# Optimization experiments

Measured on AMD Instinct MI355X. Metric: run time of the kernel, lower is better.

## Reference

```python
import jax, jax.numpy as jnp
import numpy as np

B, C, H, W = 4, 256, 64, 64
CQK = C // 8  # qk_downscale = 8


def setup_inputs() -> dict:
    key = jax.random.key(0)
    ks = jax.random.split(key, 4)
    scale = 0.02
    x = jax.random.normal(ks[0], (B, C, H, W), dtype=jnp.float32)
    Wq = jax.random.normal(ks[1], (CQK, C), dtype=jnp.float32) * scale
    bq = jnp.zeros((CQK,), dtype=jnp.float32)
    Wk = jax.random.normal(ks[2], (CQK, C), dtype=jnp.float32) * scale
    bk = jnp.zeros((CQK,), dtype=jnp.float32)
    Wv = jax.random.normal(ks[3], (C, C), dtype=jnp.float32) * scale
    bv = jnp.zeros((C,), dtype=jnp.float32)
    gamma = jnp.ones((1,), dtype=jnp.float32)
    return {"x": x, "Wq": Wq, "bq": bq, "Wk": Wk, "bk": bk,
            "Wv": Wv, "bv": bv, "gamma": gamma}


def reference(x, Wq, bq, Wk, bk, Wv, bv, gamma):
    b, c, h, w = x.shape
    n = h * w
    xf = x.reshape(b, c, n)                                   # [B,C,N]
    # 1x1 Conv1d == per-position linear projection
    q = jnp.einsum('oc,bcn->bon', Wq, xf) + bq[:, None]        # [B,C/8,N]
    k = jnp.einsum('oc,bcn->bon', Wk, xf) + bk[:, None]        # [B,C/8,N]
    v = jnp.einsum('oc,bcn->bon', Wv, xf) + bv[:, None]        # [B,C,N]
    # scores[b,i,j] = sum_c q[b,c,i] * k[b,c,j]  (bmm(q^T, k))
    scores = jnp.einsum('bci,bcj->bij', q, k)                  # [B,N,N]
    # softmax over dim=1 (the i / contracted axis) — SAGAN style, no 1/sqrt(d)
    attn = jax.nn.softmax(scores, axis=1)                      # [B,N,N]
    out = gamma * jnp.einsum('bcn,bnm->bcm', v, attn) + xf     # [B,C,N]
    return out.reshape(b, c, h, w)
```

## Files before the change

### kernel.cpp

```cpp
#include <hip/hip_runtime.h>
#include <stdint.h>

typedef __attribute__((ext_vector_type(8))) short short8;
typedef __attribute__((ext_vector_type(4))) float f32x4;
typedef __attribute__((ext_vector_type(4))) unsigned int u32x4;

#define MFMA16(a, b, c) __builtin_amdgcn_mfma_f32_16x16x32_bf16((a), (b), (c), 0, 0, 0)

#define GLOAD_LDS16(gsrc, ldst)                                                        \
    __builtin_amdgcn_global_load_lds(                                                  \
        (const __attribute__((address_space(1))) unsigned int*)(gsrc),                 \
        (__attribute__((address_space(3))) unsigned int*)(ldst), 16, 0, 0)

#define LOG2E 1.4426950408889634f

static __device__ __forceinline__ unsigned short f2bf(float f) {
    union { float f; unsigned int u; } v; v.f = f;
    unsigned int u = v.u;
    unsigned int r = 0x7fffu + ((u >> 16) & 1u);
    return (unsigned short)((u + r) >> 16);
}

static __device__ __forceinline__ float bf2f(unsigned short s) {
    union { unsigned int u; float f; } v; v.u = ((unsigned int)s) << 16;
    return v.f;
}

static __device__ __forceinline__ unsigned int cvt_pk_bf16(float lo, float hi) {
    unsigned int r;
    asm("v_cvt_pk_bf16_f32 %0, %1, %2" : "=v"(r) : "v"(lo), "v"(hi));
    return r;
}

__global__ __launch_bounds__(256) void k_prepw(const float* __restrict__ Wq,
                                               const float* __restrict__ Wk,
                                               const float* __restrict__ Wv,
                                               unsigned short* __restrict__ Wb) {
    const int i = (blockIdx.x * 256 + threadIdx.x) * 4;
    const float* src; int off;
    if (i < 8192)       { src = Wq; off = i; }
    else if (i < 16384) { src = Wk; off = i - 8192; }
    else                { src = Wv; off = i - 16384; }
    const float4 v = *(const float4*)(src + off);
    ushort4 o;
    o.x = f2bf(v.x); o.y = f2bf(v.y); o.z = f2bf(v.z); o.w = f2bf(v.w);
    *(ushort4*)(Wb + i) = o;
}

__global__ __launch_bounds__(256) void k_qkv(const float* __restrict__ x,
                                             const unsigned short* __restrict__ Wb,
                                             const float* __restrict__ bq,
                                             const float* __restrict__ bk,
                                             const float* __restrict__ bv,
                                             unsigned short* __restrict__ qT,
                                             unsigned short* __restrict__ kT,
                                             unsigned short* __restrict__ vp) {
    const int b = blockIdx.y;
    const int nt = blockIdx.x;
    const int h = blockIdx.z;
    const int lane = threadIdx.x & 63;
    const int wv = threadIdx.x >> 6;
    const int l15 = lane & 15, g = lane >> 4;
    const int n0 = nt * 64;
    const int nw = n0 + wv * 16;

    const float* xb = x + (size_t)b * 1048576;
    const float* xs = xb + (size_t)(g * 8) * 4096 + nw + l15;

    const unsigned short* Wqb = Wb;
    const unsigned short* Wkb = Wb + 8192;
    const unsigned short* Wvb = Wb + 16384 + h * 32768;

    f32x4 aqk[4] = {};
    f32x4 av[8] = {};

#pragma unroll 2
    for (int k0 = 0; k0 < 256; k0 += 32) {
        const float* xp = xs + (size_t)k0 * 4096;
        float xv[8];
#pragma unroll
        for (int j = 0; j < 8; ++j) xv[j] = xp[(size_t)j * 4096];
        const u32x4 ux = {cvt_pk_bf16(xv[0], xv[1]), cvt_pk_bf16(xv[2], xv[3]),
                          cvt_pk_bf16(xv[4], xv[5]), cvt_pk_bf16(xv[6], xv[7])};
        const short8 xa = __builtin_bit_cast(short8, ux);

        if (h == 0) {
#pragma unroll
            for (int ot = 0; ot < 4; ++ot) {
                const unsigned short* wr = (ot < 2) ? (Wqb + (size_t)(ot * 16 + l15) * 256)
                                                    : (Wkb + (size_t)((ot - 2) * 16 + l15) * 256);
                const short8 wb8 = *(const short8*)(wr + k0 + g * 8);
                aqk[ot] = MFMA16(xa, wb8, aqk[ot]);
            }
        }
#pragma unroll
        for (int ct = 0; ct < 8; ++ct) {
            const short8 wv8 = *(const short8*)(Wvb + (size_t)(ct * 16 + l15) * 256 + k0 + g * 8);
            av[ct] = MFMA16(wv8, xa, av[ct]);
        }
    }

    if (h == 0) {
#pragma unroll
        for (int ot = 0; ot < 4; ++ot) {
            const int o = (ot & 1) * 16 + l15;
            const float bias = (ot < 2) ? bq[o] : bk[o];
            const float sc = (ot < 2) ? LOG2E : 1.0f;
            unsigned short* dst = (ot < 2) ? qT : kT;
#pragma unroll
            for (int r = 0; r < 4; ++r) {
                const int n = nw + g * 4 + r;
                dst[((size_t)b * 4096 + n) * 32 + o] = f2bf((aqk[ot][r] + bias) * sc);
            }
        }
    }
    const int jp = ((wv >> 1) * 4 + (l15 >> 2)) * 8 + (wv & 1) * 4 + (l15 & 3);
#pragma unroll
    for (int ct = 0; ct < 8; ++ct)
#pragma unroll
        for (int r = 0; r < 4; ++r) {
            const int c = h * 128 + ct * 16 + g * 4 + r;
            vp[((size_t)b * 256 + c) * 4096 + n0 + jp] = f2bf(av[ct][r] + bv[c]);
        }
}

__global__ __launch_bounds__(256, 2) void k_attn(const unsigned short* __restrict__ qT,
                                                 const unsigned short* __restrict__ kT,
                                                 const unsigned short* __restrict__ vp,
                                                 unsigned short* __restrict__ Opart,
                                                 float* __restrict__ mll,
                                                 int ilen) {
    __shared__ __align__(16) unsigned short vlds[2 * 16384];

    const int b = blockIdx.y;
    const int mt = blockIdx.x;
    const int sp = blockIdx.z;
    const int tid = threadIdx.x;
    const int lane = tid & 63;
    const int wv = tid >> 6;
    const int l15 = lane & 15, g = lane >> 4;
    const int m_base = mt * 128 + wv * 32;
    const int i_start = sp * ilen;
    const int T = ilen >> 6;

    const unsigned short* qTb = qT + (size_t)b * 131072;
    const unsigned short* vpb = vp + (size_t)b * 1048576;

    const short8 qkB0 = *(const short8*)(kT + ((size_t)b * 4096 + m_base + l15) * 32 + g * 8);
    const short8 qkB1 = *(const short8*)(kT + ((size_t)b * 4096 + m_base + 16 + l15) * 32 + g * 8);

    const int jd = (lane & 7) ^ ((lane >> 3) & 7);
    const unsigned short* vsrc = vpb + (size_t)(64 * wv + (lane >> 3)) * 4096 + i_start + jd * 8;
    const int ldst0 = wv * 4096;

#define STAGE(bufsel, ioff)                                                             \
    do {                                                                                \
        _Pragma("unroll")                                                               \
        for (int s_ = 0; s_ < 8; ++s_)                                                  \
            GLOAD_LDS16(vsrc + (size_t)s_ * 32768 + (ioff),                             \
                        vlds + (bufsel) * 16384 + ldst0 + s_ * 512);                    \
    } while (0)

    const int rdA = l15 * 64 + ((g ^ (l15 & 7)) << 3);
    const int rdB = l15 * 64 + (((4 + g) ^ (l15 & 7)) << 3);

    const unsigned short* qp = qTb + (size_t)(i_start + l15) * 32 + g * 8;

    f32x4 oacc[16][2] = {};
    float l_acc0 = 0.0f, l_acc1 = 0.0f;
    const f32x4 zf = {0.f, 0.f, 0.f, 0.f};

    STAGE(0, 0);
    __syncthreads();

    for (int t = 0; t < T; ++t) {
        const int cur = t & 1;
        if (t + 1 < T) STAGE(cur ^ 1, (t + 1) * 64);

        const short8 a0 = *(const short8*)(qp);
        const short8 a1 = *(const short8*)(qp + 512);
        const short8 a2 = *(const short8*)(qp + 1024);
        const short8 a3 = *(const short8*)(qp + 1536);
        qp += 2048;
        f32x4 P[4][2];
        P[0][0] = MFMA16(a0, qkB0, zf); P[0][1] = MFMA16(a0, qkB1, zf);
        P[1][0] = MFMA16(a1, qkB0, zf); P[1][1] = MFMA16(a1, qkB1, zf);
        P[2][0] = MFMA16(a2, qkB0, zf); P[2][1] = MFMA16(a2, qkB1, zf);
        P[3][0] = MFMA16(a3, qkB0, zf); P[3][1] = MFMA16(a3, qkB1, zf);

        float s00 = 0.f, s01 = 0.f, s10 = 0.f, s11 = 0.f;
#pragma unroll
        for (int it = 0; it < 4; ++it)
#pragma unroll
            for (int r = 0; r < 4; ++r) {
                P[it][0][r] = exp2f(P[it][0][r]);
                P[it][1][r] = exp2f(P[it][1][r]);
                if (it < 2) { s00 += P[it][0][r]; s01 += P[it][1][r]; }
                else        { s10 += P[it][0][r]; s11 += P[it][1][r]; }
            }
        l_acc0 += s00 + s10;
        l_acc1 += s01 + s11;

        const u32x4 u00 = {cvt_pk_bf16(P[0][0][0], P[0][0][1]), cvt_pk_bf16(P[0][0][2], P[0][0][3]),
                           cvt_pk_bf16(P[1][0][0], P[1][0][1]), cvt_pk_bf16(P[1][0][2], P[1][0][3])};
        const u32x4 u01 = {cvt_pk_bf16(P[0][1][0], P[0][1][1]), cvt_pk_bf16(P[0][1][2], P[0][1][3]),
                           cvt_pk_bf16(P[1][1][0], P[1][1][1]), cvt_pk_bf16(P[1][1][2], P[1][1][3])};
        const u32x4 u10 = {cvt_pk_bf16(P[2][0][0], P[2][0][1]), cvt_pk_bf16(P[2][0][2], P[2][0][3]),
                           cvt_pk_bf16(P[3][0][0], P[3][0][1]), cvt_pk_bf16(P[3][0][2], P[3][0][3])};
        const u32x4 u11 = {cvt_pk_bf16(P[2][1][0], P[2][1][1]), cvt_pk_bf16(P[2][1][2], P[2][1][3]),
                           cvt_pk_bf16(P[3][1][0], P[3][1][1]), cvt_pk_bf16(P[3][1][2], P[3][1][3])};
        const short8 pb00 = __builtin_bit_cast(short8, u00);
        const short8 pb01 = __builtin_bit_cast(short8, u01);
        const short8 pb10 = __builtin_bit_cast(short8, u10);
        const short8 pb11 = __builtin_bit_cast(short8, u11);

        const unsigned short* vbase = vlds + cur * 16384;
        const unsigned short* pA = vbase + rdA;
        const unsigned short* pB = vbase + rdB;
        __builtin_amdgcn_s_setprio(1);
#pragma unroll
        for (int ct = 0; ct < 16; ++ct) {
            const short8 va0 = *(const short8*)(pA + ct * 1024);
            const short8 va1 = *(const short8*)(pB + ct * 1024);
            oacc[ct][0] = MFMA16(va0, pb00, oacc[ct][0]);
            oacc[ct][1] = MFMA16(va0, pb01, oacc[ct][1]);
            oacc[ct][0] = MFMA16(va1, pb10, oacc[ct][0]);
            oacc[ct][1] = MFMA16(va1, pb11, oacc[ct][1]);
        }
        __builtin_amdgcn_s_setprio(0);

        if (t + 1 < T) __syncthreads();
    }
#undef STAGE

    unsigned short* Ob = Opart + (size_t)(sp * 4 + b) * 1048576;
#pragma unroll
    for (int ct = 0; ct < 16; ++ct)
#pragma unroll
        for (int r = 0; r < 4; ++r) {
            const int c = ct * 16 + g * 4 + r;
            Ob[(size_t)c * 4096 + m_base + l15]      = f2bf(oacc[ct][0][r]);
            Ob[(size_t)c * 4096 + m_base + 16 + l15] = f2bf(oacc[ct][1][r]);
        }
    float l0 = l_acc0, l1 = l_acc1;
    l0 += __shfl_xor(l0, 16); l0 += __shfl_xor(l0, 32);
    l1 += __shfl_xor(l1, 16); l1 += __shfl_xor(l1, 32);
    if (lane < 16) {
        const size_t mi = (size_t)(sp * 4 + b) * 4096 + m_base + l15;
        mll[mi]      = l0;
        mll[mi + 16] = l1;
    }
}

__global__ __launch_bounds__(256) void k_combine(const unsigned short* __restrict__ Opart,
                                                 const float* __restrict__ mll,
                                                 const float* __restrict__ x,
                                                 const float* __restrict__ gamma,
                                                 float* __restrict__ out, int S) {
    const size_t e0 = ((size_t)blockIdx.x * 256 + threadIdx.x) * 8;
    const int m0 = (int)(e0 & 4095);
    const int b = (int)(e0 >> 20);

    float L[8] = {}, O[8] = {};
    for (int s = 0; s < S; ++s) {
        const size_t base = (size_t)(s * 4 + b) * 4096 + m0;
        const float4 la = *(const float4*)(mll + base);
        const float4 lc = *(const float4*)(mll + base + 4);
        const short8 op = *(const short8*)(Opart + (size_t)s * 4194304 + e0);
        L[0] += la.x; O[0] += bf2f((unsigned short)op[0]);
        L[1] += la.y; O[1] += bf2f((unsigned short)op[1]);
        L[2] += la.z; O[2] += bf2f((unsigned short)op[2]);
        L[3] += la.w; O[3] += bf2f((unsigned short)op[3]);
        L[4] += lc.x; O[4] += bf2f((unsigned short)op[4]);
        L[5] += lc.y; O[5] += bf2f((unsigned short)op[5]);
        L[6] += lc.z; O[6] += bf2f((unsigned short)op[6]);
        L[7] += lc.w; O[7] += bf2f((unsigned short)op[7]);
    }

    const float g0 = gamma[0];
    const float4 x0 = *(const float4*)(x + e0);
    const float4 x1 = *(const float4*)(x + e0 + 4);
    float4 o0, o1;
    o0.x = g0 * O[0] / L[0] + x0.x; o0.y = g0 * O[1] / L[1] + x0.y;
    o0.z = g0 * O[2] / L[2] + x0.z; o0.w = g0 * O[3] / L[3] + x0.w;
    o1.x = g0 * O[4] / L[4] + x1.x; o1.y = g0 * O[5] / L[5] + x1.y;
    o1.z = g0 * O[6] / L[6] + x1.z; o1.w = g0 * O[7] / L[7] + x1.w;
    *(float4*)(out + e0) = o0;
    *(float4*)(out + e0 + 4) = o1;
}

extern "C" void kernel_launch(void* const* d_in, const int* in_sizes, int n_in,
                              void* d_out, int out_size, void* d_ws, size_t ws_size,
                              hipStream_t stream) {
    (void)in_sizes; (void)n_in; (void)out_size;
    const float* x     = (const float*)d_in[0];
    const float* Wq    = (const float*)d_in[1];
    const float* bq    = (const float*)d_in[2];
    const float* Wk    = (const float*)d_in[3];
    const float* bk    = (const float*)d_in[4];
    const float* Wv    = (const float*)d_in[5];
    const float* bv    = (const float*)d_in[6];
    const float* gamma = (const float*)d_in[7];
    float* out = (float*)d_out;

    unsigned short* qT = (unsigned short*)d_ws;
    unsigned short* kT = qT + (size_t)4 * 4096 * 32;
    unsigned short* vp = kT + (size_t)4 * 4096 * 32;
    unsigned short* Wb = vp + (size_t)4 * 256 * 4096;
    unsigned short* Opart = Wb + 81920;

    const size_t base_el = 2 * (size_t)4 * 4096 * 32 + (size_t)4 * 256 * 4096 + 81920;
    auto need = [&](int s) {
        return (base_el + (size_t)s * 4194304) * 2 + (size_t)s * 16384 * 4;
    };
    const int S = (need(4) <= ws_size) ? 4 : (need(2) <= ws_size) ? 2 : 1;
    float* mll = (float*)(Opart + (size_t)S * 4194304);

    k_prepw<<<dim3(80), 256, 0, stream>>>(Wq, Wk, Wv, Wb);
    k_qkv<<<dim3(64, 4, 2), 256, 0, stream>>>(x, Wb, bq, bk, bv, qT, kT, vp);
    k_attn<<<dim3(32, 4, S), 256, 0, stream>>>(qT, kT, vp, Opart, mll, 4096 / S);
    k_combine<<<dim3(2048), 256, 0, stream>>>(Opart, mll, x, gamma, out, S);
}
```

Measured before the change: 93.19 us.

## Software-pipeline QK/softmax of next tile under PV MFMAs of current tile

Restructures the attention loop into a two-stage software pipeline, unrolled by two with ping-pong P buffers. The QK MFMAs and exp/pack for tile t+1 are issued around the PV MFMAs of tile t, so the exp work can overlap matrix-core work. It also drops the s_setprio calls. The loop now assumes T is even, and keeping two packed P sets live raises register pressure.

```diff
diff --git a/kernel.cpp b/kernel.cpp
--- a/kernel.cpp
+++ b/kernel.cpp
@@ -164,74 +164,95 @@
     const int rdA = l15 * 64 + ((g ^ (l15 & 7)) << 3);
     const int rdB = l15 * 64 + (((4 + g) ^ (l15 & 7)) << 3);
 
-    const unsigned short* qp = qTb + (size_t)(i_start + l15) * 32 + g * 8;
-
     f32x4 oacc[16][2] = {};
     float l_acc0 = 0.0f, l_acc1 = 0.0f;
     const f32x4 zf = {0.f, 0.f, 0.f, 0.f};
 
+#define QK_TILE(TT, P)                                                                  \
+    do {                                                                                \
+        const unsigned short* q_ = qTb + (size_t)(i_start + (TT) * 64 + l15) * 32 + g * 8; \
+        const short8 a0_ = *(const short8*)(q_);                                        \
+        const short8 a1_ = *(const short8*)(q_ + 512);                                  \
+        const short8 a2_ = *(const short8*)(q_ + 1024);                                 \
+        const short8 a3_ = *(const short8*)(q_ + 1536);                                 \
+        P[0][0] = MFMA16(a0_, qkB0, zf); P[0][1] = MFMA16(a0_, qkB1, zf);               \
+        P[1][0] = MFMA16(a1_, qkB0, zf); P[1][1] = MFMA16(a1_, qkB1, zf);               \
+        P[2][0] = MFMA16(a2_, qkB0, zf); P[2][1] = MFMA16(a2_, qkB1, zf);               \
+        P[3][0] = MFMA16(a3_, qkB0, zf); P[3][1] = MFMA16(a3_, qkB1, zf);               \
+    } while (0)
+
+#define SM_PACK(P, PB)                                                                  \
+    do {                                                                                \
+        float s00 = 0.f, s01 = 0.f, s10 = 0.f, s11 = 0.f;                               \
+        _Pragma("unroll")                                                               \
+        for (int it = 0; it < 4; ++it)                                                  \
+            _Pragma("unroll")                                                           \
+            for (int r = 0; r < 4; ++r) {                                               \
+                P[it][0][r] = exp2f(P[it][0][r]);                                       \
+                P[it][1][r] = exp2f(P[it][1][r]);                                       \
+                if (it < 2) { s00 += P[it][0][r]; s01 += P[it][1][r]; }                 \
+                else        { s10 += P[it][0][r]; s11 += P[it][1][r]; }                 \
+            }                                                                           \
+        l_acc0 += s00 + s10;                                                            \
+        l_acc1 += s01 + s11;                                                            \
+        const u32x4 u0_ = {cvt_pk_bf16(P[0][0][0], P[0][0][1]), cvt_pk_bf16(P[0][0][2], P[0][0][3]), \
+                           cvt_pk_bf16(P[1][0][0], P[1][0][1]), cvt_pk_bf16(P[1][0][2], P[1][0][3])}; \
+        const u32x4 u1_ = {cvt_pk_bf16(P[0][1][0], P[0][1][1]), cvt_pk_bf16(P[0][1][2], P[0][1][3]), \
+                           cvt_pk_bf16(P[1][1][0], P[1][1][1]), cvt_pk_bf16(P[1][1][2], P[1][1][3])}; \
+        const u32x4 u2_ = {cvt_pk_bf16(P[2][0][0], P[2][0][1]), cvt_pk_bf16(P[2][0][2], P[2][0][3]), \
+                           cvt_pk_bf16(P[3][0][0], P[3][0][1]), cvt_pk_bf16(P[3][0][2], P[3][0][3])}; \
+        const u32x4 u3_ = {cvt_pk_bf16(P[2][1][0], P[2][1][1]), cvt_pk_bf16(P[2][1][2], P[2][1][3]), \
+                           cvt_pk_bf16(P[3][1][0], P[3][1][1]), cvt_pk_bf16(P[3][1][2], P[3][1][3])}; \
+        PB[0] = __builtin_bit_cast(short8, u0_);                                        \
+        PB[1] = __builtin_bit_cast(short8, u1_);                                        \
+        PB[2] = __builtin_bit_cast(short8, u2_);                                        \
+        PB[3] = __builtin_bit_cast(short8, u3_);                                        \
+    } while (0)
+
+#define PV_TILE(CUR, PB)                                                                \
+    do {                                                                                \
+        const unsigned short* pA_ = vlds + (CUR) * 16384 + rdA;                         \
+        const unsigned short* pB_ = vlds + (CUR) * 16384 + rdB;                         \
+        _Pragma("unroll")                                                               \
+        for (int ct = 0; ct < 16; ++ct) {                                               \
+            const short8 va0_ = *(const short8*)(pA_ + ct * 1024);                      \
+            const short8 va1_ = *(const short8*)(pB_ + ct * 1024);                      \
+            oacc[ct][0] = MFMA16(va0_, PB[0], oacc[ct][0]);                             \
+            oacc[ct][1] = MFMA16(va0_, PB[1], oacc[ct][1]);                             \
+            oacc[ct][0] = MFMA16(va1_, PB[2], oacc[ct][0]);                             \
+            oacc[ct][1] = MFMA16(va1_, PB[3], oacc[ct][1]);                             \
+        }                                                                               \
+    } while (0)
+
+    short8 pbA[4], pbB[4];
+    f32x4 Pt[4][2];
+
     STAGE(0, 0);
+    QK_TILE(0, Pt);
+    SM_PACK(Pt, pbA);
     __syncthreads();
 
-    for (int t = 0; t < T; ++t) {
-        const int cur = t & 1;
-        if (t + 1 < T) STAGE(cur ^ 1, (t + 1) * 64);
-
-        const short8 a0 = *(const short8*)(qp);
-        const short8 a1 = *(const short8*)(qp + 512);
-        const short8 a2 = *(const short8*)(qp + 1024);
-        const short8 a3 = *(const short8*)(qp + 1536);
-        qp += 2048;
-        f32x4 P[4][2];
-        P[0][0] = MFMA16(a0, qkB0, zf); P[0][1] = MFMA16(a0, qkB1, zf);
-        P[1][0] = MFMA16(a1, qkB0, zf); P[1][1] = MFMA16(a1, qkB1, zf);
-        P[2][0] = MFMA16(a2, qkB0, zf); P[2][1] = MFMA16(a2, qkB1, zf);
-        P[3][0] = MFMA16(a3, qkB0, zf); P[3][1] = MFMA16(a3, qkB1, zf);
-
-        float s00 = 0.f, s01 = 0.f, s10 = 0.f, s11 = 0.f;
-#pragma unroll
-        for (int it = 0; it < 4; ++it)
-#pragma unroll
-            for (int r = 0; r < 4; ++r) {
-                P[it][0][r] = exp2f(P[it][0][r]);
-                P[it][1][r] = exp2f(P[it][1][r]);
-                if (it < 2) { s00 += P[it][0][r]; s01 += P[it][1][r]; }
-                else        { s10 += P[it][0][r]; s11 += P[it][1][r]; }
-            }
-        l_acc0 += s00 + s10;
-        l_acc1 += s01 + s11;
-
-        const u32x4 u00 = {cvt_pk_bf16(P[0][0][0], P[0][0][1]), cvt_pk_bf16(P[0][0][2], P[0][0][3]),
-                           cvt_pk_bf16(P[1][0][0], P[1][0][1]), cvt_pk_bf16(P[1][0][2], P[1][0][3])};
-        const u32x4 u01 = {cvt_pk_bf16(P[0][1][0], P[0][1][1]), cvt_pk_bf16(P[0][1][2], P[0][1][3]),
-                           cvt_pk_bf16(P[1][1][0], P[1][1][1]), cvt_pk_bf16(P[1][1][2], P[1][1][3])};
-        const u32x4 u10 = {cvt_pk_bf16(P[2][0][0], P[2][0][1]), cvt_pk_bf16(P[2][0][2], P[2][0][3]),
-                           cvt_pk_bf16(P[3][0][0], P[3][0][1]), cvt_pk_bf16(P[3][0][2], P[3][0][3])};
-        const u32x4 u11 = {cvt_pk_bf16(P[2][1][0], P[2][1][1]), cvt_pk_bf16(P[2][1][2], P[2][1][3]),
-                           cvt_pk_bf16(P[3][1][0], P[3][1][1]), cvt_pk_bf16(P[3][1][2], P[3][1][3])};
-        const short8 pb00 = __builtin_bit_cast(short8, u00);
-        const short8 pb01 = __builtin_bit_cast(short8, u01);
-        const short8 pb10 = __builtin_bit_cast(short8, u10);
-        const short8 pb11 = __builtin_bit_cast(short8, u11);
-
-        const unsigned short* vbase = vlds + cur * 16384;
-        const unsigned short* pA = vbase + rdA;
-        const unsigned short* pB = vbase + rdB;
-        __builtin_amdgcn_s_setprio(1);
-#pragma unroll
-        for (int ct = 0; ct < 16; ++ct) {
-            const short8 va0 = *(const short8*)(pA + ct * 1024);
-            const short8 va1 = *(const short8*)(pB + ct * 1024);
-            oacc[ct][0] = MFMA16(va0, pb00, oacc[ct][0]);
-            oacc[ct][1] = MFMA16(va0, pb01, oacc[ct][1]);
-            oacc[ct][0] = MFMA16(va1, pb10, oacc[ct][0]);
-            oacc[ct][1] = MFMA16(va1, pb11, oacc[ct][1]);
-        }
-        __builtin_amdgcn_s_setprio(0);
-
-        if (t + 1 < T) __syncthreads();
+    for (int t = 0; t < T; t += 2) {
+        STAGE(1, (t + 1) * 64);
+        QK_TILE(t + 1, Pt);
+        PV_TILE(0, pbA);
+        SM_PACK(Pt, pbB);
+        __syncthreads();
+
+        if (t + 2 < T) {
+            STAGE(0, (t + 2) * 64);
+            QK_TILE(t + 2, Pt);
+        }
+        PV_TILE(1, pbB);
+        if (t + 2 < T) {
+            SM_PACK(Pt, pbA);
+            __syncthreads();
+        }
     }
 #undef STAGE
+#undef QK_TILE
+#undef SM_PACK
+#undef PV_TILE
 
     unsigned short* Ob = Opart + (size_t)(sp * 4 + b) * 1048576;
 #pragma unroll
```

After: 91.46 us. About the same (-1.9%).

## Split attention waves across channel halves with 64 columns each, use native exp2

Applied to the files above, without the earlier changes.

Each wave in the attention kernel now covers 64 output columns and one half of the 256 channels, where before it covered 32 columns and all channels. This halves the LDS reads of V per wave and doubles reuse of each V fragment across MFMAs. The cost is that both waves in a pair compute the same QK scores and exponentials. The change also switches to the hardware exp2 builtin and drops the setprio hints.

```diff
diff --git a/kernel.cpp b/kernel.cpp
--- a/kernel.cpp
+++ b/kernel.cpp
@@ -30,6 +30,14 @@
     unsigned int r;
     asm("v_cvt_pk_bf16_f32 %0, %1, %2" : "=v"(r) : "v"(lo), "v"(hi));
     return r;
+}
+
+static __device__ __forceinline__ float fexp2(float x) {
+#if __has_builtin(__builtin_amdgcn_exp2f)
+    return __builtin_amdgcn_exp2f(x);
+#else
+    return exp2f(x);
+#endif
 }
 
 __global__ __launch_bounds__(256) void k_prepw(const float* __restrict__ Wq,
@@ -138,16 +146,19 @@
     const int tid = threadIdx.x;
     const int lane = tid & 63;
     const int wv = tid >> 6;
+    const int mg = wv >> 1, ch = wv & 1;
     const int l15 = lane & 15, g = lane >> 4;
-    const int m_base = mt * 128 + wv * 32;
+    const int m_base = mt * 128 + mg * 64;
     const int i_start = sp * ilen;
     const int T = ilen >> 6;
 
     const unsigned short* qTb = qT + (size_t)b * 131072;
     const unsigned short* vpb = vp + (size_t)b * 1048576;
 
-    const short8 qkB0 = *(const short8*)(kT + ((size_t)b * 4096 + m_base + l15) * 32 + g * 8);
-    const short8 qkB1 = *(const short8*)(kT + ((size_t)b * 4096 + m_base + 16 + l15) * 32 + g * 8);
+    short8 qkB[4];
+#pragma unroll
+    for (int ms = 0; ms < 4; ++ms)
+        qkB[ms] = *(const short8*)(kT + ((size_t)b * 4096 + m_base + ms * 16 + l15) * 32 + g * 8);
 
     const int jd = (lane & 7) ^ ((lane >> 3) & 7);
     const unsigned short* vsrc = vpb + (size_t)(64 * wv + (lane >> 3)) * 4096 + i_start + jd * 8;
@@ -161,13 +172,14 @@
                         vlds + (bufsel) * 16384 + ldst0 + s_ * 512);                    \
     } while (0)
 
-    const int rdA = l15 * 64 + ((g ^ (l15 & 7)) << 3);
-    const int rdB = l15 * 64 + (((4 + g) ^ (l15 & 7)) << 3);
+    const int vbase0 = ch * 8192 + l15 * 64;
+    const int slotA = (g ^ (l15 & 7)) << 3;
+    const int slotB = ((4 + g) ^ (l15 & 7)) << 3;
 
     const unsigned short* qp = qTb + (size_t)(i_start + l15) * 32 + g * 8;
 
-    f32x4 oacc[16][2] = {};
-    float l_acc0 = 0.0f, l_acc1 = 0.0f;
+    f32x4 oacc[8][4] = {};
+    float ls0 = 0.f, ls1 = 0.f, ls2 = 0.f, ls3 = 0.f;
     const f32x4 zf = {0.f, 0.f, 0.f, 0.f};
 
     STAGE(0, 0);
@@ -182,52 +194,48 @@
         const short8 a2 = *(const short8*)(qp + 1024);
         const short8 a3 = *(const short8*)(qp + 1536);
         qp += 2048;
-        f32x4 P[4][2];
-        P[0][0] = MFMA16(a0, qkB0, zf); P[0][1] = MFMA16(a0, qkB1, zf);
-        P[1][0] = MFMA16(a1, qkB0, zf); P[1][1] = MFMA16(a1, qkB1, zf);
-        P[2][0] = MFMA16(a2, qkB0, zf); P[2][1] = MFMA16(a2, qkB1, zf);
-        P[3][0] = MFMA16(a3, qkB0, zf); P[3][1] = MFMA16(a3, qkB1, zf);
-
-        float s00 = 0.f, s01 = 0.f, s10 = 0.f, s11 = 0.f;
-#pragma unroll
-        for (int it = 0; it < 4; ++it)
+
+        short8 pb0[4], pb1[4];
+#pragma unroll
+        for (int ms = 0; ms < 4; ++ms) {
+            f32x4 P0 = MFMA16(a0, qkB[ms], zf);
+            f32x4 P1 = MFMA16(a1, qkB[ms], zf);
+            f32x4 P2 = MFMA16(a2, qkB[ms], zf);
+            f32x4 P3 = MFMA16(a3, qkB[ms], zf);
+            float s = 0.f;
 #pragma unroll
             for (int r = 0; r < 4; ++r) {
-                P[it][0][r] = exp2f(P[it][0][r]);
-                P[it][1][r] = exp2f(P[it][1][r]);
-                if (it < 2) { s00 += P[it][0][r]; s01 += P[it][1][r]; }
-                else        { s10 += P[it][0][r]; s11 += P[it][1][r]; }
+                P0[r] = fexp2(P0[r]); s += P0[r];
+                P1[r] = fexp2(P1[r]); s += P1[r];
+                P2[r] = fexp2(P2[r]); s += P2[r];
+                P3[r] = fexp2(P3[r]); s += P3[r];
             }
-        l_acc0 += s00 + s10;
-        l_acc1 += s01 + s11;
-
-        const u32x4 u00 = {cvt_pk_bf16(P[0][0][0], P[0][0][1]), cvt_pk_bf16(P[0][0][2], P[0][0][3]),
-                           cvt_pk_bf16(P[1][0][0], P[1][0][1]), cvt_pk_bf16(P[1][0][2], P[1][0][3])};
-        const u32x4 u01 = {cvt_pk_bf16(P[0][1][0], P[0][1][1]), cvt_pk_bf16(P[0][1][2], P[0][1][3]),
-                           cvt_pk_bf16(P[1][1][0], P[1][1][1]), cvt_pk_bf16(P[1][1][2], P[1][1][3])};
-        const u32x4 u10 = {cvt_pk_bf16(P[2][0][0], P[2][0][1]), cvt_pk_bf16(P[2][0][2], P[2][0][3]),
-                           cvt_pk_bf16(P[3][0][0], P[3][0][1]), cvt_pk_bf16(P[3][0][2], P[3][0][3])};
-        const u32x4 u11 = {cvt_pk_bf16(P[2][1][0], P[2][1][1]), cvt_pk_bf16(P[2][1][2], P[2][1][3]),
-                           cvt_pk_bf16(P[3][1][0], P[3][1][1]), cvt_pk_bf16(P[3][1][2], P[3][1][3])};
-        const short8 pb00 = __builtin_bit_cast(short8, u00);
-        const short8 pb01 = __builtin_bit_cast(short8, u01);
-        const short8 pb10 = __builtin_bit_cast(short8, u10);
-        const short8 pb11 = __builtin_bit_cast(short8, u11);
-
-        const unsigned short* vbase = vlds + cur * 16384;
-        const unsigned short* pA = vbase + rdA;
-        const unsigned short* pB = vbase + rdB;
-        __builtin_amdgcn_s_setprio(1);
-#pragma unroll
-        for (int ct = 0; ct < 16; ++ct) {
-            const short8 va0 = *(const short8*)(pA + ct * 1024);
-            const short8 va1 = *(const short8*)(pB + ct * 1024);
-            oacc[ct][0] = MFMA16(va0, pb00, oacc[ct][0]);
-            oacc[ct][1] = MFMA16(va0, pb01, oacc[ct][1]);
-            oacc[ct][0] = MFMA16(va1, pb10, oacc[ct][0]);
-            oacc[ct][1] = MFMA16(va1, pb11, oacc[ct][1]);
-        }
-        __builtin_amdgcn_s_setprio(0);
+            if (ms == 0) ls0 += s;
+            else if (ms == 1) ls1 += s;
+            else if (ms == 2) ls2 += s;
+            else ls3 += s;
+            const u32x4 ua = {cvt_pk_bf16(P0[0], P0[1]), cvt_pk_bf16(P0[2], P0[3]),
+                              cvt_pk_bf16(P1[0], P1[1]), cvt_pk_bf16(P1[2], P1[3])};
+            const u32x4 ub = {cvt_pk_bf16(P2[0], P2[1]), cvt_pk_bf16(P2[2], P2[3]),
+                              cvt_pk_bf16(P3[0], P3[1]), cvt_pk_bf16(P3[2], P3[3])};
+            pb0[ms] = __builtin_bit_cast(short8, ua);
+            pb1[ms] = __builtin_bit_cast(short8, ub);
+        }
+
+        const unsigned short* vb = vlds + cur * 16384 + vbase0;
+#pragma unroll
+        for (int ct = 0; ct < 8; ++ct) {
+            const short8 va0 = *(const short8*)(vb + ct * 1024 + slotA);
+            const short8 va1 = *(const short8*)(vb + ct * 1024 + slotB);
+            oacc[ct][0] = MFMA16(va0, pb0[0], oacc[ct][0]);
+            oacc[ct][1] = MFMA16(va0, pb0[1], oacc[ct][1]);
+            oacc[ct][2] = MFMA16(va0, pb0[2], oacc[ct][2]);
+            oacc[ct][3] = MFMA16(va0, pb0[3], oacc[ct][3]);
+            oacc[ct][0] = MFMA16(va1, pb1[0], oacc[ct][0]);
+            oacc[ct][1] = MFMA16(va1, pb1[1], oacc[ct][1]);
+            oacc[ct][2] = MFMA16(va1, pb1[2], oacc[ct][2]);
+            oacc[ct][3] = MFMA16(va1, pb1[3], oacc[ct][3]);
+        }
 
         if (t + 1 < T) __syncthreads();
     }
@@ -235,20 +243,25 @@
 
     unsigned short* Ob = Opart + (size_t)(sp * 4 + b) * 1048576;
 #pragma unroll
-    for (int ct = 0; ct < 16; ++ct)
-#pragma unroll
-        for (int r = 0; r < 4; ++r) {
-            const int c = ct * 16 + g * 4 + r;
-            Ob[(size_t)c * 4096 + m_base + l15]      = f2bf(oacc[ct][0][r]);
-            Ob[(size_t)c * 4096 + m_base + 16 + l15] = f2bf(oacc[ct][1][r]);
-        }
-    float l0 = l_acc0, l1 = l_acc1;
+    for (int ct = 0; ct < 8; ++ct)
+#pragma unroll
+        for (int ms = 0; ms < 4; ++ms)
+#pragma unroll
+            for (int r = 0; r < 4; ++r) {
+                const int c = ch * 128 + ct * 16 + g * 4 + r;
+                Ob[(size_t)c * 4096 + m_base + ms * 16 + l15] = f2bf(oacc[ct][ms][r]);
+            }
+    float l0 = ls0, l1 = ls1, l2 = ls2, l3 = ls3;
     l0 += __shfl_xor(l0, 16); l0 += __shfl_xor(l0, 32);
     l1 += __shfl_xor(l1, 16); l1 += __shfl_xor(l1, 32);
-    if (lane < 16) {
+    l2 += __shfl_xor(l2, 16); l2 += __shfl_xor(l2, 32);
+    l3 += __shfl_xor(l3, 16); l3 += __shfl_xor(l3, 32);
+    if (ch == 0 && lane < 16) {
         const size_t mi = (size_t)(sp * 4 + b) * 4096 + m_base + l15;
         mll[mi]      = l0;
         mll[mi + 16] = l1;
+        mll[mi + 32] = l2;
+        mll[mi + 48] = l3;
     }
 }
 
```

New measurement: 113.2 us. +21.5%, slower.
